# Kernel optimization log

Measured on AMD Instinct MI355X. Metric: run time of the kernel, lower is better.

Reference implementation:

```python
import jax, jax.numpy as jnp
import numpy as np

PC_RANGE = (-140.8, -40.0, -3.0, 140.8, 40.0, 1.0)
VOX = (0.4, 0.4, 4.0)
H_GRID = 200   # (40 - (-40)) / 0.4
W_GRID = 704   # (140.8 - (-140.8)) / 0.4
C = 256        # embed_dim
N_BOX = 128
BN_EPS = 1e-5


def _make_boxes(key, n):
    # Realistic CCW-ordered 3D box corners (bottom 4 first, matching pred_box[:, :4, :2]).
    k1, k2, k3, k4, k5 = jax.random.split(key, 5)
    cx = jax.random.uniform(k1, (n,), minval=PC_RANGE[0] + 10.0, maxval=PC_RANGE[3] - 10.0)
    cy = jax.random.uniform(k2, (n,), minval=PC_RANGE[1] + 5.0, maxval=PC_RANGE[4] - 5.0)
    L = jax.random.uniform(k3, (n,), minval=2.0, maxval=8.0)
    Wd = jax.random.uniform(k4, (n,), minval=1.0, maxval=3.0)
    yaw = jax.random.uniform(k5, (n,), minval=0.0, maxval=2.0 * np.pi)
    # CCW offsets: (+l,+w), (-l,+w), (-l,-w), (+l,-w)
    ox = jnp.stack([L, -L, -L, L], axis=1) * 0.5   # [n,4]
    oy = jnp.stack([Wd, Wd, -Wd, -Wd], axis=1) * 0.5
    c, s = jnp.cos(yaw)[:, None], jnp.sin(yaw)[:, None]
    px = c * ox - s * oy + cx[:, None]
    py = s * ox + c * oy + cy[:, None]
    bot = jnp.stack([px, py, jnp.full_like(px, -1.0)], axis=-1)  # [n,4,3]
    top = jnp.stack([px, py, jnp.full_like(px, 1.0)], axis=-1)
    return jnp.concatenate([bot, top], axis=1)  # [n,8,3]


def setup_inputs() -> dict:
    key = jax.random.key(0)
    ks = jax.random.split(key, 16)
    inp = {
        "pred_box": _make_boxes(ks[0], N_BOX),
        "pred_score": jax.random.uniform(ks[1], (N_BOX,)),
        # MLP: Linear(25,C) -> ReLU -> Linear(C,C) -> ReLU -> Linear(C,C)
        "w1": jax.random.normal(ks[2], (25, C)) * 0.1,
        "b1": jnp.zeros((C,)),
        "w2": jax.random.normal(ks[3], (C, C)) * 0.05,
        "b2": jnp.zeros((C,)),
        "w3": jax.random.normal(ks[4], (C, C)) * 0.05,
        "b3": jnp.zeros((C,)),
        # 3 refine blocks x 2 convs, OIHW
        "conv_w": jax.random.normal(ks[5], (3, 2, C, C, 3, 3)) * 0.02,
        "bn_gamma": 1.0 + 0.1 * jax.random.normal(ks[6], (3, 2, C)),
        "bn_beta": 0.1 * jax.random.normal(ks[7], (3, 2, C)),
        "bn_mean": 0.1 * jax.random.normal(ks[8], (3, 2, C)),
        "bn_var": jax.random.uniform(ks[9], (3, 2, C), minval=0.5, maxval=1.5),
    }
    return inp


def _conv(x, w):
    return jax.lax.conv_general_dilated(
        x, w, window_strides=(1, 1), padding="SAME",
        dimension_numbers=("NCHW", "OIHW", "NCHW"))


def _bn(x, g, b, m, v):
    inv = g / jnp.sqrt(v + BN_EPS)
    return x * inv[None, :, None, None] + (b - m * inv)[None, :, None, None]


def reference(pred_box, pred_score, w1, b1, w2, b2, w3, b3,
              conv_w, bn_gamma, bn_beta, bn_mean, bn_var):
    n = pred_box.shape[0]
    # per-box feature: MLP(corners flattened + score) * score
    feat = jnp.concatenate([pred_box.reshape(n, -1), pred_score[:, None]], axis=1)  # [N,25]
    h = jax.nn.relu(feat @ w1 + b1)
    h = jax.nn.relu(h @ w2 + b2)
    obj = (h @ w3 + b3) * pred_score[:, None]  # [N,C]

    xmin, ymin = PC_RANGE[0], PC_RANGE[1]
    dx, dy = VOX[0], VOX[1]
    gx = (pred_box[:, :4, 0] - xmin) / dx  # [N,4] polygon verts in grid units
    gy = (pred_box[:, :4, 1] - ymin) / dy
    cxs = jnp.arange(W_GRID, dtype=pred_box.dtype) + 0.5  # cell centers
    cys = jnp.arange(H_GRID, dtype=pred_box.dtype) + 0.5

    # point-in-quad via 4 edge cross products (all >= 0 for CCW polygon)
    inside = jnp.ones((n, H_GRID, W_GRID), dtype=bool)
    for e in range(4):
        ax, ay = gx[:, e], gy[:, e]
        bx, by = gx[:, (e + 1) % 4], gy[:, (e + 1) % 4]
        vx, vy = bx - ax, by - ay
        c = (vx[:, None, None] * (cys[None, :, None] - ay[:, None, None])
             - vy[:, None, None] * (cxs[None, None, :] - ax[:, None, None]))  # [N,H,W]
        inside = inside & (c >= 0)
    insf = inside.astype(obj.dtype)

    feat_sum = jnp.einsum("nhw,nc->chw", insf, obj)        # masked scatter-add
    feat_cnt = jnp.maximum(insf.sum(axis=0), 1.0)           # [H,W]
    x = (feat_sum / feat_cnt[None])[None]                   # [1,C,H,W]

    for blk in range(3):
        res = x
        y = jax.nn.relu(_bn(_conv(x, conv_w[blk, 0]),
                            bn_gamma[blk, 0], bn_beta[blk, 0], bn_mean[blk, 0], bn_var[blk, 0]))
        y = _bn(_conv(y, conv_w[blk, 1]),
                bn_gamma[blk, 1], bn_beta[blk, 1], bn_mean[blk, 1], bn_var[blk, 1])
        x = jax.nn.relu(y + res)
    return x[0]  # [C,H,W]
```

## Files before the change

kernel.cpp:

```cpp
#include <hip/hip_runtime.h>

#define HG 200
#define WGR 704
#define CC 256
#define NBOX 128

typedef unsigned short u16;
typedef __attribute__((ext_vector_type(8))) short short8;
typedef __attribute__((ext_vector_type(4))) short short4v;
typedef __attribute__((ext_vector_type(4))) float floatx4;

typedef __attribute__((address_space(1))) const unsigned int guint;
typedef __attribute__((address_space(3))) unsigned int luint;

__device__ __forceinline__ float bf2f(u16 u) {
  unsigned int x = ((unsigned int)u) << 16;
  return __builtin_bit_cast(float, x);
}
__device__ __forceinline__ u16 f2bf(float f) {
  unsigned int x = __builtin_bit_cast(unsigned int, f);
  x += 0x7fffu + ((x >> 16) & 1u);
  return (u16)(x >> 16);
}

__global__ __launch_bounds__(256) void pack_w_kernel(const float* __restrict__ cw, u16* __restrict__ W2) {
  int i = blockIdx.x * 256 + threadIdx.x;
  int conv = i / 589824;
  int r = i - conv * 589824;
  int tap = r / 65536;
  int r2 = r - tap * 65536;
  int ck = r2 >> 13;
  int r3 = r2 & 8191;
  int cogrp = r3 >> 9;
  int r4 = r3 & 511;
  int lane = r4 >> 3;
  int j = r4 & 7;
  int co = cogrp * 16 + (lane & 15);
  int ci = ck * 32 + (lane >> 4) * 8 + j;
  W2[i] = f2bf(cw[((conv * 256 + co) * 256 + ci) * 9 + tap]);
}

__global__ __launch_bounds__(256) void bn_prep_kernel(const float* __restrict__ g, const float* __restrict__ b,
                                                      const float* __restrict__ m, const float* __restrict__ v,
                                                      float* __restrict__ binv, float* __restrict__ bbias) {
  int i = blockIdx.x * 256 + threadIdx.x;
  float inv = g[i] / sqrtf(v[i] + 1e-5f);
  binv[i] = inv;
  bbias[i] = b[i] - m[i] * inv;
}

__global__ __launch_bounds__(128) void box_prep_kernel(const float* __restrict__ pb, float* __restrict__ geo) {
  int b = threadIdx.x;
  float gx[4], gy[4];
#pragma unroll
  for (int j = 0; j < 4; ++j) {
    float px = pb[(b * 8 + j) * 3 + 0];
    float py = pb[(b * 8 + j) * 3 + 1];
    gx[j] = __fdiv_rn(__fsub_rn(px, -140.8f), 0.4f);
    gy[j] = __fdiv_rn(__fsub_rn(py, -40.0f), 0.4f);
  }
  float* g = geo + b * 16;
#pragma unroll
  for (int e = 0; e < 4; ++e) {
    g[e * 4 + 0] = gx[e];
    g[e * 4 + 1] = gy[e];
    g[e * 4 + 2] = __fsub_rn(gx[(e + 1) & 3], gx[e]);
    g[e * 4 + 3] = __fsub_rn(gy[(e + 1) & 3], gy[e]);
  }
}

__global__ __launch_bounds__(256) void mlp_kernel(
    const float* __restrict__ pb, const float* __restrict__ score,
    const float* __restrict__ w1, const float* __restrict__ b1,
    const float* __restrict__ w2, const float* __restrict__ b2,
    const float* __restrict__ w3, const float* __restrict__ b3,
    float* __restrict__ obj) {
  __shared__ float sf[25];
  __shared__ float h1[256];
  __shared__ float h2[256];
  int b = blockIdx.x, t = threadIdx.x;
  if (t < 24) sf[t] = pb[b * 24 + t];
  if (t == 24) sf[24] = score[b];
  __syncthreads();
  float a = b1[t];
  for (int k = 0; k < 25; ++k) a += sf[k] * w1[k * 256 + t];
  h1[t] = fmaxf(a, 0.0f);
  __syncthreads();
  a = b2[t];
  for (int k = 0; k < 256; ++k) a += h1[k] * w2[k * 256 + t];
  h2[t] = fmaxf(a, 0.0f);
  __syncthreads();
  a = b3[t];
  for (int k = 0; k < 256; ++k) a += h2[k] * w3[k * 256 + t];
  obj[b * 256 + t] = a * score[b];
}

__global__ __launch_bounds__(256) void raster_kernel(
    const float* __restrict__ geo, const float* __restrict__ obj, u16* __restrict__ x0) {
  __shared__ float sG[NBOX * 17];
  int tid = threadIdx.x;
  for (int i = tid; i < NBOX * 16; i += 256) sG[(i >> 4) * 17 + (i & 15)] = geo[i];
  __syncthreads();
  int wid = tid >> 6, lane = tid & 63;
  int cell = blockIdx.x * 4 + wid;
  int h = cell / WGR, w = cell - h * WGR;
  float cx = w + 0.5f, cy = h + 0.5f;

  auto test = [&](int n) -> bool {
    const float* g = &sG[n * 17];
    bool ok = true;
#pragma unroll
    for (int e = 0; e < 4; ++e) {
      float ax = g[e * 4 + 0], ay = g[e * 4 + 1];
      float vx = g[e * 4 + 2], vy = g[e * 4 + 3];
      float c = __fsub_rn(__fmul_rn(vx, __fsub_rn(cy, ay)),
                          __fmul_rn(vy, __fsub_rn(cx, ax)));
      ok = ok && (c >= 0.0f);
    }
    return ok;
  };

  unsigned long long m0 = __ballot(test(lane));
  unsigned long long m1 = __ballot(test(lane + 64));
  int cnt = __popcll(m0) + __popcll(m1);
  floatx4 s = {0.f, 0.f, 0.f, 0.f};
  while (m0) { int n = __builtin_ctzll(m0); m0 &= m0 - 1; s += *(const floatx4*)(obj + n * CC + lane * 4); }
  while (m1) { int n = 64 + __builtin_ctzll(m1); m1 &= m1 - 1; s += *(const floatx4*)(obj + n * CC + lane * 4); }
  float cf = fmaxf((float)cnt, 1.0f);
  short4v o;
#pragma unroll
  for (int j = 0; j < 4; ++j) o[j] = (short)f2bf(__fdiv_rn(s[j], cf));
  *(short4v*)(x0 + cell * CC + lane * 4) = o;
}

template <bool ADD_RES>
__global__ __launch_bounds__(256, 3) void conv_kernel(
    const u16* __restrict__ in, const u16* __restrict__ wgt,
    const float* __restrict__ bninv, const float* __restrict__ bnbias,
    const u16* __restrict__ res, u16* __restrict__ out) {
  __shared__ u16 sA[2 * 1056 * 8];

  const int w0 = blockIdx.x * 64;
  const int h0 = blockIdx.y * 2;
  const int c0g = blockIdx.z * 8;
  const int tid = threadIdx.x;
  const int lane = tid & 63;
  const int wid = tid >> 6;
  const int ln15 = lane & 15;
  const int quad = lane >> 4;
  const int mi = wid >> 1;
  const int ni = wid & 1;

  const u16* ga[5];
  bool gv[5];
#pragma unroll
  for (int j = 0; j < 5; ++j) {
    int I = wid + 4 * j;
    int s = I * 64 + lane;
    int r = s / 264;
    int rem = s - r * 264;
    int q = rem / 66;
    int px = rem - q * 66;
    int gh = h0 + r - 1;
    int gw = w0 + px - 1;
    bool ok = (I <= 16) && (s < 1056) &&
              ((unsigned)gh < (unsigned)HG) && ((unsigned)gw < (unsigned)WGR);
    ga[j] = in + (gh * WGR + gw) * CC + q * 8;
    gv[j] = ok;
    if (I <= 16 && s < 1056 && !ok) {
      short8 z = {};
      *(short8*)(&sA[s * 8]) = z;
      *(short8*)(&sA[(1056 + s) * 8]) = z;
    }
  }

  auto dma = [&](int buf) {
#pragma unroll
    for (int j = 0; j < 5; ++j) {
      int I = wid + 4 * j;
      if (I <= 16) {
        u16* lp = &sA[buf * 8448 + I * 512];
        if (gv[j])
          __builtin_amdgcn_global_load_lds((guint*)(const void*)ga[j], (luint*)(void*)lp, 16, 0, 0);
      }
      ga[j] += 32;
    }
  };

  const u16* wbase = wgt + ((size_t)(c0g + ni * 4)) * 512 + lane * 8;
  auto loadB = [&](int ck, int tap, short8* dst) {
#pragma unroll
    for (int nt = 0; nt < 4; ++nt)
      dst[nt] = *(const short8*)(wbase + ((tap * 8 + ck) * 16 + nt) * 512);
  };

  floatx4 acc[4][4] = {};
  short8 A[2][4];
  short8 B[2][4];
  dma(0);

  for (int ck = 0; ck < 8; ++ck) {
    const int cur = ck & 1;
    __syncthreads();
    loadB(ck, 0, B[0]);
    loadB(ck, 1, B[1]);
    if (ck < 7) dma(1 - cur);

    const u16* base = &sA[cur * 8448];
#pragma unroll
    for (int mt = 0; mt < 4; ++mt)
      A[0][mt] = *(const short8*)(base + ((mi * 4 + quad) * 66 + mt * 16 + ln15) * 8);

#pragma unroll
    for (int t = 0; t < 9; ++t) {
      if (t < 8) {
        const int kh = (t + 1) / 3;
        const int kw = (t + 1) - kh * 3;
#pragma unroll
        for (int mt = 0; mt < 4; ++mt)
          A[(t + 1) & 1][mt] =
              *(const short8*)(base + (((mi + kh) * 4 + quad) * 66 + mt * 16 + ln15 + kw) * 8);
        if (t >= 1) loadB(ck, t + 1, B[(t + 1) & 1]);
      }
      const short8* ac = A[t & 1];
      const short8* bc = B[t & 1];
      __builtin_amdgcn_s_setprio(1);
#pragma unroll
      for (int mt = 0; mt < 4; ++mt)
#pragma unroll
        for (int nt = 0; nt < 4; ++nt)
          acc[mt][nt] = __builtin_amdgcn_mfma_f32_16x16x32_bf16(ac[mt], bc[nt], acc[mt][nt], 0, 0, 0);
      __builtin_amdgcn_s_setprio(0);
    }
  }

  const int h = h0 + mi;
  float binv[4], bbia[4];
#pragma unroll
  for (int nt = 0; nt < 4; ++nt) {
    int co = (c0g + ni * 4 + nt) * 16 + ln15;
    binv[nt] = bninv[co];
    bbia[nt] = bnbias[co];
  }

#pragma unroll
  for (int mt = 0; mt < 4; ++mt) {
#pragma unroll
    for (int nt = 0; nt < 4; ++nt) {
      int co = (c0g + ni * 4 + nt) * 16 + ln15;
#pragma unroll
      for (int r = 0; r < 4; ++r) {
        int w = w0 + mt * 16 + quad * 4 + r;
        int idx = (h * WGR + w) * CC + co;
        float v = acc[mt][nt][r] * binv[nt] + bbia[nt];
        if (ADD_RES) v += bf2f(res[idx]);
        v = fmaxf(v, 0.0f);
        out[idx] = f2bf(v);
      }
    }
  }
}

__global__ __launch_bounds__(256) void transpose_kernel(const u16* __restrict__ src, float* __restrict__ dst) {
  __shared__ u16 sT[64][68];
  int w0 = blockIdx.x * 64, h = blockIdx.y, c0 = blockIdx.z * 64;
  int tid = threadIdx.x;
  int cl = (tid & 15) * 4, wl = tid >> 4;
#pragma unroll
  for (int i = 0; i < 4; ++i) {
    int w = wl + i * 16;
    short4v v = *(const short4v*)(src + (h * WGR + w0 + w) * CC + c0 + cl);
    *(short4v*)(&sT[w][cl]) = v;
  }
  __syncthreads();
  int w4 = (tid & 15) * 4, ch = tid >> 4;
#pragma unroll
  for (int i = 0; i < 4; ++i) {
    int c = ch + i * 16;
    floatx4 v;
    v[0] = bf2f(sT[w4 + 0][c]);
    v[1] = bf2f(sT[w4 + 1][c]);
    v[2] = bf2f(sT[w4 + 2][c]);
    v[3] = bf2f(sT[w4 + 3][c]);
    *(floatx4*)(dst + (size_t)(c0 + c) * (HG * WGR) + h * WGR + w0 + w4) = v;
  }
}

extern "C" void kernel_launch(void* const* d_in, const int* in_sizes, int n_in,
                              void* d_out, int out_size, void* d_ws, size_t ws_size,
                              hipStream_t stream) {
  const float* pred_box = (const float*)d_in[0];
  const float* pred_score = (const float*)d_in[1];
  const float* w1 = (const float*)d_in[2];
  const float* b1 = (const float*)d_in[3];
  const float* w2 = (const float*)d_in[4];
  const float* b2 = (const float*)d_in[5];
  const float* w3 = (const float*)d_in[6];
  const float* b3 = (const float*)d_in[7];
  const float* conv_w = (const float*)d_in[8];
  const float* bng = (const float*)d_in[9];
  const float* bnb = (const float*)d_in[10];
  const float* bnm = (const float*)d_in[11];
  const float* bnv = (const float*)d_in[12];

  char* ws = (char*)d_ws;
  u16* W2       = (u16*)(ws);
  u16* Abuf     = (u16*)(ws + 7077888);
  float* obj    = (float*)(ws + 79167488);
  float* bninv  = (float*)(ws + 79298560);
  float* bnbias = (float*)(ws + 79304704);
  float* geo    = (float*)(ws + 79310848);
  u16* SCR = (u16*)d_out;
  float* OUT = (float*)d_out;

  pack_w_kernel<<<13824, 256, 0, stream>>>(conv_w, W2);
  bn_prep_kernel<<<6, 256, 0, stream>>>(bng, bnb, bnm, bnv, bninv, bnbias);
  box_prep_kernel<<<1, 128, 0, stream>>>(pred_box, geo);
  mlp_kernel<<<NBOX, 256, 0, stream>>>(pred_box, pred_score, w1, b1, w2, b2, w3, b3, obj);
  raster_kernel<<<35200, 256, 0, stream>>>(geo, obj, Abuf);

  dim3 cg(11, 100, 2);
  conv_kernel<false><<<cg, 256, 0, stream>>>(Abuf, W2 + 0 * 589824, bninv + 0 * 256, bnbias + 0 * 256, nullptr, SCR);
  conv_kernel<true ><<<cg, 256, 0, stream>>>(SCR,  W2 + 1 * 589824, bninv + 1 * 256, bnbias + 1 * 256, Abuf, Abuf);
  conv_kernel<false><<<cg, 256, 0, stream>>>(Abuf, W2 + 2 * 589824, bninv + 2 * 256, bnbias + 2 * 256, nullptr, SCR);
  conv_kernel<true ><<<cg, 256, 0, stream>>>(SCR,  W2 + 3 * 589824, bninv + 3 * 256, bnbias + 3 * 256, Abuf, Abuf);
  conv_kernel<false><<<cg, 256, 0, stream>>>(Abuf, W2 + 4 * 589824, bninv + 4 * 256, bnbias + 4 * 256, nullptr, SCR);
  conv_kernel<true ><<<cg, 256, 0, stream>>>(SCR,  W2 + 5 * 589824, bninv + 5 * 256, bnbias + 5 * 256, Abuf, Abuf);
  transpose_kernel<<<dim3(11, HG, 4), 256, 0, stream>>>(Abuf, OUT);
}
```

Before: 1.118 ms.

## Compute two output rows per wave in conv kernel to reuse weight fragments

The conv block tile grows from 2 to 4 output rows, so each wave now accumulates two rows with separate accumulators while sharing each loaded weight fragment across both. The staged LDS input tile grows to 6 rows and the grid halves along H. The aim is to halve weight traffic per MFMA and cut halo reloads. In exchange it doubles accumulator registers and LDS use, so occupancy drops to 2 blocks per CU.

```diff
diff --git a/kernel.cpp b/kernel.cpp
--- a/kernel.cpp
+++ b/kernel.cpp
@@ -134,27 +134,27 @@
 }
 
 template <bool ADD_RES>
-__global__ __launch_bounds__(256, 3) void conv_kernel(
+__global__ __launch_bounds__(256, 2) void conv_kernel(
     const u16* __restrict__ in, const u16* __restrict__ wgt,
     const float* __restrict__ bninv, const float* __restrict__ bnbias,
     const u16* __restrict__ res, u16* __restrict__ out) {
-  __shared__ u16 sA[2 * 1056 * 8];
+  __shared__ u16 sA[2 * 1584 * 8];
 
   const int w0 = blockIdx.x * 64;
-  const int h0 = blockIdx.y * 2;
+  const int h0 = blockIdx.y * 4;
   const int c0g = blockIdx.z * 8;
   const int tid = threadIdx.x;
   const int lane = tid & 63;
   const int wid = tid >> 6;
   const int ln15 = lane & 15;
   const int quad = lane >> 4;
-  const int mi = wid >> 1;
+  const int rp = wid >> 1;
   const int ni = wid & 1;
 
-  const u16* ga[5];
-  bool gv[5];
-#pragma unroll
-  for (int j = 0; j < 5; ++j) {
+  const u16* ga[7];
+  bool gv[7];
+#pragma unroll
+  for (int j = 0; j < 7; ++j) {
     int I = wid + 4 * j;
     int s = I * 64 + lane;
     int r = s / 264;
@@ -163,23 +163,23 @@
     int px = rem - q * 66;
     int gh = h0 + r - 1;
     int gw = w0 + px - 1;
-    bool ok = (I <= 16) && (s < 1056) &&
+    bool ok = (I <= 24) && (s < 1584) &&
               ((unsigned)gh < (unsigned)HG) && ((unsigned)gw < (unsigned)WGR);
     ga[j] = in + (gh * WGR + gw) * CC + q * 8;
     gv[j] = ok;
-    if (I <= 16 && s < 1056 && !ok) {
+    if (I <= 24 && s < 1584 && !ok) {
       short8 z = {};
       *(short8*)(&sA[s * 8]) = z;
-      *(short8*)(&sA[(1056 + s) * 8]) = z;
+      *(short8*)(&sA[(1584 + s) * 8]) = z;
     }
   }
 
   auto dma = [&](int buf) {
 #pragma unroll
-    for (int j = 0; j < 5; ++j) {
+    for (int j = 0; j < 7; ++j) {
       int I = wid + 4 * j;
-      if (I <= 16) {
-        u16* lp = &sA[buf * 8448 + I * 512];
+      if (I <= 24) {
+        u16* lp = &sA[buf * 12672 + I * 512];
         if (gv[j])
           __builtin_amdgcn_global_load_lds((guint*)(const void*)ga[j], (luint*)(void*)lp, 16, 0, 0);
       }
@@ -194,8 +194,9 @@
       dst[nt] = *(const short8*)(wbase + ((tap * 8 + ck) * 16 + nt) * 512);
   };
 
-  floatx4 acc[4][4] = {};
-  short8 A[2][4];
+  floatx4 acc0[4][4] = {};
+  floatx4 acc1[4][4] = {};
+  short8 A0[4], A1[4];
   short8 B[2][4];
   dma(0);
 
@@ -206,35 +207,43 @@
     loadB(ck, 1, B[1]);
     if (ck < 7) dma(1 - cur);
 
-    const u16* base = &sA[cur * 8448];
+    const u16* base = &sA[cur * 12672];
 #pragma unroll
     for (int mt = 0; mt < 4; ++mt)
-      A[0][mt] = *(const short8*)(base + ((mi * 4 + quad) * 66 + mt * 16 + ln15) * 8);
+      A0[mt] = *(const short8*)(base + (((rp * 2) * 4 + quad) * 66 + mt * 16 + ln15) * 8);
 
 #pragma unroll
     for (int t = 0; t < 9; ++t) {
+      const int kh = t / 3;
+      const int kw = t - kh * 3;
+#pragma unroll
+      for (int mt = 0; mt < 4; ++mt)
+        A1[mt] = *(const short8*)(base + (((rp * 2 + 1 + kh) * 4 + quad) * 66 + mt * 16 + ln15 + kw) * 8);
+      __builtin_amdgcn_s_setprio(1);
+#pragma unroll
+      for (int mt = 0; mt < 4; ++mt)
+#pragma unroll
+        for (int nt = 0; nt < 4; ++nt)
+          acc0[mt][nt] = __builtin_amdgcn_mfma_f32_16x16x32_bf16(A0[mt], B[t & 1][nt], acc0[mt][nt], 0, 0, 0);
+      __builtin_amdgcn_s_setprio(0);
       if (t < 8) {
-        const int kh = (t + 1) / 3;
-        const int kw = (t + 1) - kh * 3;
+        const int kh2 = (t + 1) / 3;
+        const int kw2 = (t + 1) - kh2 * 3;
 #pragma unroll
         for (int mt = 0; mt < 4; ++mt)
-          A[(t + 1) & 1][mt] =
-              *(const short8*)(base + (((mi + kh) * 4 + quad) * 66 + mt * 16 + ln15 + kw) * 8);
-        if (t >= 1) loadB(ck, t + 1, B[(t + 1) & 1]);
+          A0[mt] = *(const short8*)(base + (((rp * 2 + kh2) * 4 + quad) * 66 + mt * 16 + ln15 + kw2) * 8);
       }
-      const short8* ac = A[t & 1];
-      const short8* bc = B[t & 1];
       __builtin_amdgcn_s_setprio(1);
 #pragma unroll
       for (int mt = 0; mt < 4; ++mt)
 #pragma unroll
         for (int nt = 0; nt < 4; ++nt)
-          acc[mt][nt] = __builtin_amdgcn_mfma_f32_16x16x32_bf16(ac[mt], bc[nt], acc[mt][nt], 0, 0, 0);
+          acc1[mt][nt] = __builtin_amdgcn_mfma_f32_16x16x32_bf16(A1[mt], B[t & 1][nt], acc1[mt][nt], 0, 0, 0);
       __builtin_amdgcn_s_setprio(0);
-    }
-  }
-
-  const int h = h0 + mi;
+      if (t < 7) loadB(ck, t + 2, B[t & 1]);
+    }
+  }
+
   float binv[4], bbia[4];
 #pragma unroll
   for (int nt = 0; nt < 4; ++nt) {
@@ -244,18 +253,22 @@
   }
 
 #pragma unroll
-  for (int mt = 0; mt < 4; ++mt) {
-#pragma unroll
-    for (int nt = 0; nt < 4; ++nt) {
-      int co = (c0g + ni * 4 + nt) * 16 + ln15;
-#pragma unroll
-      for (int r = 0; r < 4; ++r) {
-        int w = w0 + mt * 16 + quad * 4 + r;
-        int idx = (h * WGR + w) * CC + co;
-        float v = acc[mt][nt][r] * binv[nt] + bbia[nt];
-        if (ADD_RES) v += bf2f(res[idx]);
-        v = fmaxf(v, 0.0f);
-        out[idx] = f2bf(v);
+  for (int rr = 0; rr < 2; ++rr) {
+    const int h = h0 + rp * 2 + rr;
+#pragma unroll
+    for (int mt = 0; mt < 4; ++mt) {
+#pragma unroll
+      for (int nt = 0; nt < 4; ++nt) {
+        int co = (c0g + ni * 4 + nt) * 16 + ln15;
+#pragma unroll
+        for (int r = 0; r < 4; ++r) {
+          int w = w0 + mt * 16 + quad * 4 + r;
+          int idx = (h * WGR + w) * CC + co;
+          float v = (rr ? acc1[mt][nt][r] : acc0[mt][nt][r]) * binv[nt] + bbia[nt];
+          if (ADD_RES) v += bf2f(res[idx]);
+          v = fmaxf(v, 0.0f);
+          out[idx] = f2bf(v);
+        }
       }
     }
   }
@@ -319,7 +332,7 @@
   mlp_kernel<<<NBOX, 256, 0, stream>>>(pred_box, pred_score, w1, b1, w2, b2, w3, b3, obj);
   raster_kernel<<<35200, 256, 0, stream>>>(geo, obj, Abuf);
 
-  dim3 cg(11, 100, 2);
+  dim3 cg(11, 50, 2);
   conv_kernel<false><<<cg, 256, 0, stream>>>(Abuf, W2 + 0 * 589824, bninv + 0 * 256, bnbias + 0 * 256, nullptr, SCR);
   conv_kernel<true ><<<cg, 256, 0, stream>>>(SCR,  W2 + 1 * 589824, bninv + 1 * 256, bnbias + 1 * 256, Abuf, Abuf);
   conv_kernel<false><<<cg, 256, 0, stream>>>(Abuf, W2 + 2 * 589824, bninv + 2 * 256, bnbias + 2 * 256, nullptr, SCR);
```

Measured after the change: 1.080 ms. 1.04x faster.

## Interleave output channels in packed weights for vectorized epilogue and deeper B prefetch

Applied to the files above, without the earlier changes.

Reorders the packed weight layout so that each lane's four MFMA N-tiles cover four adjacent output channels. The epilogue can then load BN parameters and residuals and store outputs as 4-wide short vectors instead of scalar u16 accesses. The B operand now uses a triple-buffered register prefetch that runs three taps ahead and crosses into the next channel chunk, and the LDS DMA is issued after tap 2 rather than at chunk start. This adds register pressure from the extra B buffer, which may affect occupancy under launch_bounds(256,3).

```diff
diff --git a/kernel.cpp b/kernel.cpp
--- a/kernel.cpp
+++ b/kernel.cpp
@@ -31,11 +31,13 @@
   int r2 = r - tap * 65536;
   int ck = r2 >> 13;
   int r3 = r2 & 8191;
-  int cogrp = r3 >> 9;
-  int r4 = r3 & 511;
-  int lane = r4 >> 3;
-  int j = r4 & 7;
-  int co = cogrp * 16 + (lane & 15);
+  int g64 = r3 >> 11;
+  int r4 = r3 & 2047;
+  int f = r4 >> 9;
+  int r5 = r4 & 511;
+  int lane = r5 >> 3;
+  int j = r5 & 7;
+  int co = g64 * 64 + (lane & 15) * 4 + f;
   int ci = ck * 32 + (lane >> 4) * 8 + j;
   W2[i] = f2bf(cw[((conv * 256 + co) * 256 + ci) * 9 + tap]);
 }
@@ -142,7 +144,6 @@
 
   const int w0 = blockIdx.x * 64;
   const int h0 = blockIdx.y * 2;
-  const int c0g = blockIdx.z * 8;
   const int tid = threadIdx.x;
   const int lane = tid & 63;
   const int wid = tid >> 6;
@@ -150,6 +151,7 @@
   const int quad = lane >> 4;
   const int mi = wid >> 1;
   const int ni = wid & 1;
+  const int g64 = blockIdx.z * 2 + ni;
 
   const u16* ga[5];
   bool gv[5];
@@ -187,24 +189,25 @@
     }
   };
 
-  const u16* wbase = wgt + ((size_t)(c0g + ni * 4)) * 512 + lane * 8;
+  const u16* wbase = wgt + (size_t)g64 * 2048 + lane * 8;
   auto loadB = [&](int ck, int tap, short8* dst) {
 #pragma unroll
-    for (int nt = 0; nt < 4; ++nt)
-      dst[nt] = *(const short8*)(wbase + ((tap * 8 + ck) * 16 + nt) * 512);
+    for (int f = 0; f < 4; ++f)
+      dst[f] = *(const short8*)(wbase + ((tap * 8 + ck) * 16 + f) * 512);
   };
 
   floatx4 acc[4][4] = {};
   short8 A[2][4];
-  short8 B[2][4];
+  short8 B[3][4];
+
   dma(0);
+  loadB(0, 0, B[0]);
+  loadB(0, 1, B[1]);
+  loadB(0, 2, B[2]);
 
   for (int ck = 0; ck < 8; ++ck) {
     const int cur = ck & 1;
     __syncthreads();
-    loadB(ck, 0, B[0]);
-    loadB(ck, 1, B[1]);
-    if (ck < 7) dma(1 - cur);
 
     const u16* base = &sA[cur * 8448];
 #pragma unroll
@@ -220,43 +223,44 @@
         for (int mt = 0; mt < 4; ++mt)
           A[(t + 1) & 1][mt] =
               *(const short8*)(base + (((mi + kh) * 4 + quad) * 66 + mt * 16 + ln15 + kw) * 8);
-        if (t >= 1) loadB(ck, t + 1, B[(t + 1) & 1]);
       }
       const short8* ac = A[t & 1];
-      const short8* bc = B[t & 1];
+      const short8* bc = B[t % 3];
       __builtin_amdgcn_s_setprio(1);
 #pragma unroll
       for (int mt = 0; mt < 4; ++mt)
 #pragma unroll
-        for (int nt = 0; nt < 4; ++nt)
-          acc[mt][nt] = __builtin_amdgcn_mfma_f32_16x16x32_bf16(ac[mt], bc[nt], acc[mt][nt], 0, 0, 0);
+        for (int f = 0; f < 4; ++f)
+          acc[mt][f] = __builtin_amdgcn_mfma_f32_16x16x32_bf16(ac[mt], bc[f], acc[mt][f], 0, 0, 0);
       __builtin_amdgcn_s_setprio(0);
+      if (t <= 5) loadB(ck, t + 3, B[t % 3]);
+      else if (ck < 7) loadB(ck + 1, t - 6, B[t % 3]);
+      if (t == 2 && ck < 7) dma(1 - cur);
     }
   }
 
   const int h = h0 + mi;
-  float binv[4], bbia[4];
-#pragma unroll
-  for (int nt = 0; nt < 4; ++nt) {
-    int co = (c0g + ni * 4 + nt) * 16 + ln15;
-    binv[nt] = bninv[co];
-    bbia[nt] = bnbias[co];
-  }
+  const int cobase = g64 * 64 + ln15 * 4;
+  floatx4 bi = *(const floatx4*)(bninv + cobase);
+  floatx4 bb = *(const floatx4*)(bnbias + cobase);
 
 #pragma unroll
   for (int mt = 0; mt < 4; ++mt) {
 #pragma unroll
-    for (int nt = 0; nt < 4; ++nt) {
-      int co = (c0g + ni * 4 + nt) * 16 + ln15;
-#pragma unroll
-      for (int r = 0; r < 4; ++r) {
-        int w = w0 + mt * 16 + quad * 4 + r;
-        int idx = (h * WGR + w) * CC + co;
-        float v = acc[mt][nt][r] * binv[nt] + bbia[nt];
-        if (ADD_RES) v += bf2f(res[idx]);
+    for (int r = 0; r < 4; ++r) {
+      int w = w0 + mt * 16 + quad * 4 + r;
+      int idx = (h * WGR + w) * CC + cobase;
+      short4v rv;
+      if (ADD_RES) rv = *(const short4v*)(res + idx);
+      short4v o;
+#pragma unroll
+      for (int f = 0; f < 4; ++f) {
+        float v = acc[mt][f][r] * bi[f] + bb[f];
+        if (ADD_RES) v += bf2f((u16)rv[f]);
         v = fmaxf(v, 0.0f);
-        out[idx] = f2bf(v);
+        o[f] = (short)f2bf(v);
       }
+      *(short4v*)(out + idx) = o;
     }
   }
 }
```

New measurement: 1.755 ms. 56.9% more time.

## Remap conv warps to split output channels and reuse LDS A-rows across kernel rows

Applied to the files above, without the earlier changes.

Each wave now covers both output rows and 2 channel tiles (32 channels), where before it covered one row and 64 channels. A fragments are read from LDS per input row and column shift, and each one serves up to two output rows with a rotating three-buffer scheme. Weight fragments are loaded in kw-major order with triple buffering. The aim is fewer LDS reads per MFMA and better overlap of loads with compute. The next-chunk DMA is also moved to the middle of the tap loop. In exchange, the order of register rotation is more complex and B loads per MFMA may rise.

```diff
diff --git a/kernel.cpp b/kernel.cpp
--- a/kernel.cpp
+++ b/kernel.cpp
@@ -142,14 +142,12 @@
 
   const int w0 = blockIdx.x * 64;
   const int h0 = blockIdx.y * 2;
-  const int c0g = blockIdx.z * 8;
   const int tid = threadIdx.x;
   const int lane = tid & 63;
   const int wid = tid >> 6;
   const int ln15 = lane & 15;
   const int quad = lane >> 4;
-  const int mi = wid >> 1;
-  const int ni = wid & 1;
+  const int cg = blockIdx.z * 8 + wid * 2;
 
   const u16* ga[5];
   bool gv[5];
@@ -187,75 +185,100 @@
     }
   };
 
-  const u16* wbase = wgt + ((size_t)(c0g + ni * 4)) * 512 + lane * 8;
+  const u16* wbase = wgt + ((size_t)cg) * 512 + lane * 8;
   auto loadB = [&](int ck, int tap, short8* dst) {
 #pragma unroll
-    for (int nt = 0; nt < 4; ++nt)
+    for (int nt = 0; nt < 2; ++nt)
       dst[nt] = *(const short8*)(wbase + ((tap * 8 + ck) * 16 + nt) * 512);
   };
 
-  floatx4 acc[4][4] = {};
-  short8 A[2][4];
-  short8 B[2][4];
+  floatx4 acc0[4][2] = {};
+  floatx4 acc1[4][2] = {};
+  short8 Ab[3][4];
+  short8 Bp[3][2];
   dma(0);
 
   for (int ck = 0; ck < 8; ++ck) {
     const int cur = ck & 1;
     __syncthreads();
-    loadB(ck, 0, B[0]);
-    loadB(ck, 1, B[1]);
-    if (ck < 7) dma(1 - cur);
+    loadB(ck, 0, Bp[0]);
+    loadB(ck, 3, Bp[1]);
+    loadB(ck, 6, Bp[2]);
 
     const u16* base = &sA[cur * 8448];
 #pragma unroll
-    for (int mt = 0; mt < 4; ++mt)
-      A[0][mt] = *(const short8*)(base + ((mi * 4 + quad) * 66 + mt * 16 + ln15) * 8);
-
-#pragma unroll
-    for (int t = 0; t < 9; ++t) {
-      if (t < 8) {
-        const int kh = (t + 1) / 3;
-        const int kw = (t + 1) - kh * 3;
+    for (int mt = 0; mt < 4; ++mt) {
+      Ab[0][mt] = *(const short8*)(base + ((0 * 4 + quad) * 66 + mt * 16 + ln15) * 8);
+      Ab[1][mt] = *(const short8*)(base + ((1 * 4 + quad) * 66 + mt * 16 + ln15) * 8);
+      Ab[2][mt] = *(const short8*)(base + ((2 * 4 + quad) * 66 + mt * 16 + ln15) * 8);
+    }
+
+#pragma unroll
+    for (int kw = 0; kw < 3; ++kw) {
+#pragma unroll
+      for (int j = 0; j < 6; ++j) {
+        const int kh = j >> 1;
+        const int rr = j & 1;
+        const int li = kw * 4 + kh + rr;
+        const int p = kw * 3 + kh;
+        const short8* af = Ab[li % 3];
+        const short8* bf = Bp[p % 3];
+        __builtin_amdgcn_s_setprio(1);
 #pragma unroll
         for (int mt = 0; mt < 4; ++mt)
-          A[(t + 1) & 1][mt] =
-              *(const short8*)(base + (((mi + kh) * 4 + quad) * 66 + mt * 16 + ln15 + kw) * 8);
-        if (t >= 1) loadB(ck, t + 1, B[(t + 1) & 1]);
+#pragma unroll
+          for (int nt = 0; nt < 2; ++nt) {
+            if (rr == 0)
+              acc0[mt][nt] = __builtin_amdgcn_mfma_f32_16x16x32_bf16(af[mt], bf[nt], acc0[mt][nt], 0, 0, 0);
+            else
+              acc1[mt][nt] = __builtin_amdgcn_mfma_f32_16x16x32_bf16(af[mt], bf[nt], acc1[mt][nt], 0, 0, 0);
+          }
+        __builtin_amdgcn_s_setprio(0);
+        if (j == 0 || j == 2 || j == 4 || j == 5) {
+          const int ln = li + 3;
+          if (ln <= 11) {
+            const int r2 = ln & 3;
+            const int k2 = ln >> 2;
+            const int b2 = ln % 3;
+#pragma unroll
+            for (int mt = 0; mt < 4; ++mt)
+              Ab[b2][mt] = *(const short8*)(base + ((r2 * 4 + quad) * 66 + mt * 16 + ln15 + k2) * 8);
+          }
+        }
+        if (rr == 1) {
+          const int pn = p + 3;
+          if (pn <= 8) loadB(ck, (pn % 3) * 3 + pn / 3, Bp[pn % 3]);
+        }
+        if (kw == 1 && j == 5 && ck < 7) dma(1 - cur);
       }
-      const short8* ac = A[t & 1];
-      const short8* bc = B[t & 1];
-      __builtin_amdgcn_s_setprio(1);
-#pragma unroll
-      for (int mt = 0; mt < 4; ++mt)
-#pragma unroll
-        for (int nt = 0; nt < 4; ++nt)
-          acc[mt][nt] = __builtin_amdgcn_mfma_f32_16x16x32_bf16(ac[mt], bc[nt], acc[mt][nt], 0, 0, 0);
-      __builtin_amdgcn_s_setprio(0);
-    }
-  }
-
-  const int h = h0 + mi;
-  float binv[4], bbia[4];
-#pragma unroll
-  for (int nt = 0; nt < 4; ++nt) {
-    int co = (c0g + ni * 4 + nt) * 16 + ln15;
-    binv[nt] = bninv[co];
-    bbia[nt] = bnbias[co];
-  }
-
-#pragma unroll
-  for (int mt = 0; mt < 4; ++mt) {
-#pragma unroll
-    for (int nt = 0; nt < 4; ++nt) {
-      int co = (c0g + ni * 4 + nt) * 16 + ln15;
-#pragma unroll
-      for (int r = 0; r < 4; ++r) {
-        int w = w0 + mt * 16 + quad * 4 + r;
-        int idx = (h * WGR + w) * CC + co;
-        float v = acc[mt][nt][r] * binv[nt] + bbia[nt];
-        if (ADD_RES) v += bf2f(res[idx]);
-        v = fmaxf(v, 0.0f);
-        out[idx] = f2bf(v);
+    }
+  }
+
+  float binv_[2], bbia_[2];
+#pragma unroll
+  for (int nt = 0; nt < 2; ++nt) {
+    int co = (cg + nt) * 16 + ln15;
+    binv_[nt] = bninv[co];
+    bbia_[nt] = bnbias[co];
+  }
+
+#pragma unroll
+  for (int rr = 0; rr < 2; ++rr) {
+    const int h = h0 + rr;
+#pragma unroll
+    for (int mt = 0; mt < 4; ++mt) {
+#pragma unroll
+      for (int nt = 0; nt < 2; ++nt) {
+        int co = (cg + nt) * 16 + ln15;
+#pragma unroll
+        for (int r = 0; r < 4; ++r) {
+          int w = w0 + mt * 16 + quad * 4 + r;
+          int idx = (h * WGR + w) * CC + co;
+          float v = (rr ? acc1[mt][nt][r] : acc0[mt][nt][r]) * binv_[nt] + bbia_[nt];
+          if (ADD_RES) v += bf2f(res[idx]);
+          v = fmaxf(v, 0.0f);
+          out[idx] = f2bf(v);
+        }
       }
     }
   }
```

Result: slower. 1.266 ms (+13.2%).
